# Kernel optimization log

Hardware: AMD Instinct MI355X
Metric: run time of the kernel (lower is better)

Reference implementation:

```python
import jax, jax.numpy as jnp
import numpy as np

IN, OUT, RANK, ALPHA, NSUB = 4096, 4096, 16, 32, 4
SCALING = ALPHA / RANK


def setup_inputs() -> dict:
    key = jax.random.key(0)
    ks = jax.random.split(key, 8)
    B, S = 4, 2048
    return {
        "x": jax.random.normal(ks[0], (B, S, IN), dtype=jnp.float32),
        "base_W": jax.random.normal(ks[1], (OUT, IN), dtype=jnp.float32) * 0.02,
        "base_b": jax.random.normal(ks[2], (OUT,), dtype=jnp.float32) * 0.02,
        "base_A": jax.random.normal(ks[3], (RANK, IN), dtype=jnp.float32) * 0.02,
        "base_B": jax.random.normal(ks[4], (OUT, RANK), dtype=jnp.float32) * 0.02,
        "sub_wgate": jax.random.normal(ks[5], (NSUB, IN), dtype=jnp.float32) * 0.02,
        "sub_A": jax.random.normal(ks[6], (NSUB, RANK, IN), dtype=jnp.float32) * 0.02,
        "sub_B": jax.random.normal(ks[7], (NSUB, OUT, RANK), dtype=jnp.float32) * 0.02,
    }


def reference(x, base_W, base_b, base_A, base_B, sub_wgate, sub_A, sub_B):
    # base linear: [B,S,IN] @ [IN,OUT] + bias
    out = jnp.einsum("bsd,od->bso", x, base_W) + base_b
    # base LoRA: x @ A^T @ B^T
    out = out + SCALING * jnp.einsum("bsr,or->bso", jnp.einsum("bsd,rd->bsr", x, base_A), base_B)
    # stacked ReLU-gated sub-adapters, batched over adapter dim j
    gates = jax.nn.relu(jnp.einsum("bsd,jd->bsj", x, sub_wgate))        # [B,S,J]
    mid = jnp.einsum("bsd,jrd->bsjr", x, sub_A)                           # [B,S,J,R] (small)
    # gate * (mid @ B^T) == (gate*mid) @ B^T since gate is per-token scalar
    gated_mid = mid * gates[..., None]
    out = out + SCALING * jnp.einsum("bsjr,jor->bso", gated_mid, sub_B)
    return out
```

## Files before the change

kernel.cpp:

```cpp
#include <hip/hip_runtime.h>
#include <hip/hip_bf16.h>
#include <stdint.h>

#define DIN   4096
#define DOUT  4096
#define RANK  16
#define NSUB  4
#define MTOT  8192
#define LDK   4160
#define KTAIL 64
#define NV    80
#define KTILES 65

typedef __attribute__((ext_vector_type(8)))  short    short8;
typedef __attribute__((ext_vector_type(4)))  float    floatx4;
typedef __attribute__((ext_vector_type(8)))  unsigned short ushort8;
typedef __attribute__((ext_vector_type(4)))  unsigned short ushort4v;

static __device__ __forceinline__ unsigned short f2bf(float f) {
    unsigned int u = __float_as_uint(f);
    unsigned int r = (u + 0x7FFFu + ((u >> 16) & 1u)) >> 16;
    return (unsigned short)r;
}

static __device__ __forceinline__ void async_copy16(const unsigned short* g, unsigned short* l) {
    __builtin_amdgcn_global_load_lds(
        (const __attribute__((address_space(1))) unsigned int*)g,
        (__attribute__((address_space(3))) unsigned int*)l,
        16, 0, 0);
}

__global__ __launch_bounds__(256) void build_v_kernel(
    const float* __restrict__ sub_wgate,
    const float* __restrict__ sub_A,
    unsigned short* __restrict__ Vc)
{
    const int t = threadIdx.x;
    const int row = blockIdx.x;
    const float* src = (row < 64) ? (sub_A + (size_t)row * DIN)
                     : (row < 68) ? (sub_wgate + (size_t)(row - 64) * DIN)
                     : nullptr;
#pragma unroll
    for (int i = 0; i < 4; ++i) {
        int c4 = t + 256 * i;
        ushort4v v;
        if (src) {
            float4 a = ((const float4*)src)[c4];
            v[0] = f2bf(a.x); v[1] = f2bf(a.y); v[2] = f2bf(a.z); v[3] = f2bf(a.w);
        } else {
            v[0] = v[1] = v[2] = v[3] = 0;
        }
        *(ushort4v*)(Vc + (size_t)row * DIN + c4 * 4) = v;
    }
}

__global__ __launch_bounds__(256) void convert_x_kernel(
    const float* __restrict__ x,
    unsigned short* __restrict__ Xc)
{
    const int t = threadIdx.x;
    const int b = blockIdx.x;
#pragma unroll
    for (int i = 0; i < 4; ++i) {
        const int row = b * 4 + i;
        const float4* s = (const float4*)(x + (size_t)row * DIN + t * 16);
        float4 a = s[0], b4 = s[1], c = s[2], d = s[3];
        ushort8 v0, v1;
        v0[0] = f2bf(a.x);  v0[1] = f2bf(a.y);  v0[2] = f2bf(a.z);  v0[3] = f2bf(a.w);
        v0[4] = f2bf(b4.x); v0[5] = f2bf(b4.y); v0[6] = f2bf(b4.z); v0[7] = f2bf(b4.w);
        v1[0] = f2bf(c.x);  v1[1] = f2bf(c.y);  v1[2] = f2bf(c.z);  v1[3] = f2bf(c.w);
        v1[4] = f2bf(d.x);  v1[5] = f2bf(d.y);  v1[6] = f2bf(d.z);  v1[7] = f2bf(d.w);
        unsigned short* o = Xc + (size_t)row * LDK + t * 16;
        *(ushort8*)o       = v0;
        *(ushort8*)(o + 8) = v1;
    }
}

#define XS_STG(P) do { unsigned short* d_ = &lds[(P)*8192 + t*8]; \
    _Pragma("unroll") for (int i_ = 0; i_ < 4; ++i_) \
        async_copy16(pXs + (size_t)(8*i_) * LDK, d_ + i_*2048); } while (0)
#define VS_STG(P) do { unsigned short* d_ = &lds[16384 + (P)*20480 + t*8]; \
    _Pragma("unroll") for (int i_ = 0; i_ < 10; ++i_) \
        async_copy16(pVs + (size_t)(8*i_) * DIN, d_ + i_*2048); } while (0)

#define XT_MM(P, KB) do { \
    short8 a0_ = *(const short8*)((const char*)lds + (P)*16384 + aB + (KB)); \
    short8 a1_ = *(const short8*)((const char*)lds + (P)*16384 + 8192 + aB + (KB)); \
    _Pragma("unroll") for (int n_ = 0; n_ < 5; ++n_) { \
        short8 b_ = *(const short8*)((const char*)lds + 32768 + (P)*40960 + n_*8192 + aB + (KB)); \
        acc[0][n_] = __builtin_amdgcn_mfma_f32_16x16x32_bf16(a0_, b_, acc[0][n_], 0, 0, 0); \
        acc[1][n_] = __builtin_amdgcn_mfma_f32_16x16x32_bf16(a1_, b_, acc[1][n_], 0, 0, 0); } \
} while (0)

#define XT_ITER(P, WN, DOSTG) do { \
    asm volatile("s_waitcnt vmcnt(" #WN ")" ::: "memory"); \
    asm volatile("s_barrier" ::: "memory"); \
    XT_MM(P, kb0); \
    XT_MM(P, kb1); \
    asm volatile("s_barrier" ::: "memory"); \
    if (DOSTG) { XS_STG(P); VS_STG(P); } \
    pXs += 256; pVs += 256; \
} while (0)

__global__ __launch_bounds__(256) void xtail_kernel(
    const unsigned short* __restrict__ Vc,
    unsigned short* __restrict__ Xc)
{
    __shared__ __align__(16) unsigned short lds[57344];

    const int t = threadIdx.x;
    const int l = t & 63;
    const int w = t >> 6;
    const int lane16 = l & 15;
    const int g = l >> 4;
    const int lx2 = lane16 & 7;
    const int m0 = blockIdx.x * 32;

    const int srow = t >> 5;
    const int scl  = (t & 31) ^ (srow & 7);
    const unsigned short* pXs = Xc + (size_t)(m0 + srow) * LDK + scl * 8;
    const unsigned short* pVs = Vc + (size_t)srow * DIN + scl * 8;

    const int hk  = lx2 >> 2;
    const int gx  = g ^ (lx2 & 3);
    const int kb0 = (((2*w + 0) ^ hk) * 4 + gx) * 16;
    const int kb1 = (((2*w + 1) ^ hk) * 4 + gx) * 16;
    const int aB  = lane16 * 512;

    floatx4 acc[2][5] = {};

    XS_STG(0); VS_STG(0); pXs += 256; pVs += 256;
    XS_STG(1); VS_STG(1); pXs += 256; pVs += 256;

#pragma unroll 1
    for (int c = 0; c < 14; c += 2) {
        XT_ITER(0, 14, 1);
        XT_ITER(1, 14, 1);
    }
    XT_ITER(0, 14, 0);
    XT_ITER(1, 0, 0);

    float* Pp = (float*)lds;
#pragma unroll
    for (int tm = 0; tm < 2; ++tm)
#pragma unroll
        for (int n = 0; n < 5; ++n)
#pragma unroll
            for (int r = 0; r < 4; ++r)
                Pp[((w * 32) + tm * 16 + (l >> 4) * 4 + r) * 80 + n * 16 + lane16] = acc[tm][n][r];
    __syncthreads();

#pragma unroll
    for (int i = 0; i < 8; ++i) {
        int v  = t + 256 * i;
        int tr = v >> 6;
        int c  = v & 63;
        int j  = c >> 4;
        float ps = 0.f, gs = 0.f;
#pragma unroll
        for (int q = 0; q < 4; ++q) {
            ps += Pp[(q * 32 + tr) * 80 + c];
            gs += Pp[(q * 32 + tr) * 80 + 64 + j];
        }
        Xc[(size_t)(m0 + tr) * LDK + DIN + c] = f2bf(2.0f * fmaxf(gs, 0.f) * ps);
    }
}

__global__ __launch_bounds__(256) void build_w_kernel(
    const float* __restrict__ W,
    const float* __restrict__ base_A,
    const float* __restrict__ base_B,
    const float* __restrict__ sub_B,
    unsigned short* __restrict__ Wc)
{
    __shared__ float bBs[8 * RANK];

    const int t  = threadIdx.x;
    const int o0 = (blockIdx.x >> 2) * 8;
    const int cc = (blockIdx.x & 3) * 1024;
    const int q  = (cc >> 2) + t;

    if (t < 128) bBs[t] = 2.0f * base_B[(size_t)o0 * RANK + t];
    __syncthreads();

    float4 acc[8];
#pragma unroll
    for (int o = 0; o < 8; ++o)
        acc[o] = ((const float4*)(W + (size_t)(o0 + o) * DIN))[q];

#pragma unroll
    for (int r = 0; r < RANK; ++r) {
        float4 a = ((const float4*)(base_A + (size_t)r * DIN))[q];
#pragma unroll
        for (int o = 0; o < 8; ++o) {
            float s = bBs[o * RANK + r];
            acc[o].x += s * a.x; acc[o].y += s * a.y;
            acc[o].z += s * a.z; acc[o].w += s * a.w;
        }
    }

#pragma unroll
    for (int o = 0; o < 8; ++o) {
        ushort4v v;
        v[0] = f2bf(acc[o].x); v[1] = f2bf(acc[o].y);
        v[2] = f2bf(acc[o].z); v[3] = f2bf(acc[o].w);
        *(ushort4v*)(Wc + (size_t)(o0 + o) * LDK + q * 4) = v;
    }

    if ((blockIdx.x & 3) == 0) {
#pragma unroll
        for (int i = 0; i < 2; ++i) {
            int v = t + 256 * i;
            int o = v >> 6;
            int c = v & 63;
            int j = c >> 4;
            int r = c & 15;
            float s = sub_B[((size_t)j * DOUT + (o0 + o)) * RANK + r];
            Wc[(size_t)(o0 + o) * LDK + DIN + c] = f2bf(s);
        }
    }
}

#define BARM() asm volatile("s_barrier" ::: "memory")

#define LDA_(B,MH,I,S) (*(const short8*)((const char*)lds + (B)*32768 + (MH)*8192 + (I)*2048 + (aBy ^ ((S)*64))))
#define LDB_(B,J,S)    (*(const short8*)((const char*)lds + 65536 + (B)*32768 + (J)*2048 + (bBy ^ ((S)*64))))

#define STG(P, DST) do { async_copy16((P), (DST)); \
                         async_copy16((P) + (size_t)64 * LDK, (DST) + 4096); } while (0)
#define STAGE_A0(P,B) STG((P), &lds[(B)*16384 + tid*8])
#define STAGE_A1(P,B) STG((P), &lds[(B)*16384 + 8192 + tid*8])
#define STAGE_B0(P,B) STG((P), &lds[32768 + (B)*16384 + tid*8])
#define STAGE_B1(P,B) STG((P), &lds[32768 + (B)*16384 + 8192 + tid*8])

#define MFMA_HALF(MH, JLO) do { \
    _Pragma("unroll") for (int s_ = 0; s_ < 2; ++s_) \
    _Pragma("unroll") for (int i_ = 0; i_ < 4; ++i_) \
    _Pragma("unroll") for (int jj_ = 0; jj_ < 2; ++jj_) \
        acc[(MH)*4+i_][(JLO)+jj_] = __builtin_amdgcn_mfma_f32_16x16x32_bf16( \
            af[i_][s_], bb[(JLO)+jj_][s_], acc[(MH)*4+i_][(JLO)+jj_], 0, 0, 0); \
} while (0)

#define TILE_BODY(T, CUR) do { \
     \
    _Pragma("unroll") for (int i_ = 0; i_ < 4; ++i_) { \
        af[i_][0] = LDA_(CUR, 0, i_, 0); af[i_][1] = LDA_(CUR, 0, i_, 1); } \
    _Pragma("unroll") for (int j_ = 0; j_ < 2; ++j_) { \
        bb[j_][0] = LDB_(CUR, j_, 0); bb[j_][1] = LDB_(CUR, j_, 1); } \
    if ((T) + 1 < KTILES) { STAGE_A1(pA1, (CUR) ^ 1); } \
    pA1 += 64; \
    __builtin_amdgcn_s_setprio(1); MFMA_HALF(0, 0); __builtin_amdgcn_s_setprio(0); \
    BARM(); \
     \
    _Pragma("unroll") for (int j_ = 2; j_ < 4; ++j_) { \
        bb[j_][0] = LDB_(CUR, j_, 0); bb[j_][1] = LDB_(CUR, j_, 1); } \
    __builtin_amdgcn_s_setprio(1); MFMA_HALF(0, 2); __builtin_amdgcn_s_setprio(0); \
    BARM(); \
     \
    _Pragma("unroll") for (int i_ = 0; i_ < 4; ++i_) { \
        af[i_][0] = LDA_(CUR, 1, i_, 0); af[i_][1] = LDA_(CUR, 1, i_, 1); } \
    if ((T) + 2 < KTILES) { STAGE_B0(pB0, CUR); STAGE_B1(pB1, CUR); } \
    pB0 += 64; pB1 += 64; \
    BARM(); \
    if ((T) + 2 < KTILES) { STAGE_A0(pA0, CUR); } \
    pA0 += 64; \
    __builtin_amdgcn_s_setprio(1); MFMA_HALF(1, 0); MFMA_HALF(1, 2); __builtin_amdgcn_s_setprio(0); \
    if ((T) + 2 < KTILES)      { asm volatile("s_waitcnt vmcnt(6)" ::: "memory"); } \
    else if ((T) + 1 < KTILES) { asm volatile("s_waitcnt vmcnt(0)" ::: "memory"); } \
    BARM(); \
} while (0)

__global__ __launch_bounds__(512, 2) void gemm_kernel(
    const unsigned short* __restrict__ Xc,
    const unsigned short* __restrict__ Wc,
    const float* __restrict__ bias,
    float* __restrict__ out)
{
    __shared__ unsigned short lds[65536];

    const int tid = threadIdx.x;
    const int l   = tid & 63;
    const int wv  = tid >> 6;
    const int wm  = wv >> 2;
    const int wn  = wv & 3;
    const int lane16 = l & 15;
    const int g   = l >> 4;
    const int lx  = lane16 & 7;

    const int bid = blockIdx.x;
    const int wg  = (bid & 7) * 64 + (bid >> 3);
    const int m0  = (wg >> 4) * 256;
    const int n0  = (wg & 15) * 256;

    const int aBy = wm * 16384 + lane16 * 128 + ((g ^ lx) << 4);
    const int bBy = wn * 8192  + lane16 * 128 + ((g ^ lx) << 4);

    const int r0 = tid >> 3;
    const int c0 = (tid & 7) ^ (r0 & 7);
    const unsigned short* pA0 = Xc + (size_t)(m0 + r0) * LDK + c0 * 8;
    const unsigned short* pA1 = pA0 + (size_t)128 * LDK;
    const unsigned short* pB0 = Wc + (size_t)(n0 + r0) * LDK + c0 * 8;
    const unsigned short* pB1 = pB0 + (size_t)128 * LDK;

    floatx4 acc[8][4] = {};
    short8 af[4][2], bb[4][2];

    STAGE_B0(pB0, 0); STAGE_B1(pB1, 0); STAGE_A0(pA0, 0); STAGE_A1(pA1, 0);
    STAGE_B0(pB0 + 64, 1); STAGE_B1(pB1 + 64, 1); STAGE_A0(pA0 + 64, 1);
    pA1 += 64; pB0 += 128; pB1 += 128; pA0 += 128;
    asm volatile("s_waitcnt vmcnt(6)" ::: "memory");
    BARM();

    for (int t = 0; t < KTILES - 1; t += 2) {
        TILE_BODY(t, 0);
        TILE_BODY(t + 1, 1);
    }
    TILE_BODY(KTILES - 1, 0);

    const int row_l = g * 4;
#pragma unroll
    for (int j = 0; j < 4; ++j) {
        const int gcol = n0 + wn * 64 + j * 16 + lane16;
        const float bv = bias[gcol];
#pragma unroll
        for (int i = 0; i < 8; ++i) {
            const int grow = m0 + wm * 128 + i * 16 + row_l;
            size_t base = (size_t)grow * DOUT + gcol;
            out[base]            = acc[i][j][0] + bv;
            out[base + DOUT]     = acc[i][j][1] + bv;
            out[base + 2 * DOUT] = acc[i][j][2] + bv;
            out[base + 3 * DOUT] = acc[i][j][3] + bv;
        }
    }
}

extern "C" void kernel_launch(void* const* d_in, const int* in_sizes, int n_in,
                              void* d_out, int out_size, void* d_ws, size_t ws_size,
                              hipStream_t stream) {
    const float* x         = (const float*)d_in[0];
    const float* base_W    = (const float*)d_in[1];
    const float* base_b    = (const float*)d_in[2];
    const float* base_A    = (const float*)d_in[3];
    const float* base_B    = (const float*)d_in[4];
    const float* sub_wgate = (const float*)d_in[5];
    const float* sub_A     = (const float*)d_in[6];
    const float* sub_B     = (const float*)d_in[7];
    float* out = (float*)d_out;

    unsigned short* Xc = (unsigned short*)d_ws;
    unsigned short* Wc = Xc + (size_t)MTOT * LDK;
    unsigned short* Vc = Wc + (size_t)DOUT * LDK;

    build_v_kernel<<<NV, 256, 0, stream>>>(sub_wgate, sub_A, Vc);
    convert_x_kernel<<<MTOT / 4, 256, 0, stream>>>(x, Xc);
    xtail_kernel<<<MTOT / 32, 256, 0, stream>>>(Vc, Xc);
    build_w_kernel<<<(DOUT / 8) * 4, 256, 0, stream>>>(base_W, base_A, base_B, sub_B, Wc);
    gemm_kernel<<<dim3(DOUT / 256 * (MTOT / 256)), 512, 0, stream>>>(Xc, Wc, base_b, out);
}
```

Measured before the change: 530.3 us.

## Merge prep kernels into one launch and restructure GEMM tile barrier schedule

New measurement: 528.4 us. No clear change (-0.4%).

```diff
diff --git a/kernel.cpp b/kernel.cpp
--- a/kernel.cpp
+++ b/kernel.cpp
@@ -30,49 +30,99 @@
         16, 0, 0);
 }
 
-__global__ __launch_bounds__(256) void build_v_kernel(
+__global__ __launch_bounds__(256) void prep_kernel(
+    const float* __restrict__ x,
+    unsigned short* __restrict__ Xc,
     const float* __restrict__ sub_wgate,
     const float* __restrict__ sub_A,
-    unsigned short* __restrict__ Vc)
+    unsigned short* __restrict__ Vc,
+    const float* __restrict__ W,
+    const float* __restrict__ base_A,
+    const float* __restrict__ base_B,
+    const float* __restrict__ sub_B,
+    unsigned short* __restrict__ Wc)
 {
+    __shared__ float bBs[8 * RANK];
     const int t = threadIdx.x;
-    const int row = blockIdx.x;
-    const float* src = (row < 64) ? (sub_A + (size_t)row * DIN)
-                     : (row < 68) ? (sub_wgate + (size_t)(row - 64) * DIN)
-                     : nullptr;
-#pragma unroll
-    for (int i = 0; i < 4; ++i) {
-        int c4 = t + 256 * i;
-        ushort4v v;
-        if (src) {
-            float4 a = ((const float4*)src)[c4];
-            v[0] = f2bf(a.x); v[1] = f2bf(a.y); v[2] = f2bf(a.z); v[3] = f2bf(a.w);
-        } else {
-            v[0] = v[1] = v[2] = v[3] = 0;
-        }
-        *(ushort4v*)(Vc + (size_t)row * DIN + c4 * 4) = v;
-    }
-}
-
-__global__ __launch_bounds__(256) void convert_x_kernel(
-    const float* __restrict__ x,
-    unsigned short* __restrict__ Xc)
-{
-    const int t = threadIdx.x;
-    const int b = blockIdx.x;
-#pragma unroll
-    for (int i = 0; i < 4; ++i) {
-        const int row = b * 4 + i;
-        const float4* s = (const float4*)(x + (size_t)row * DIN + t * 16);
-        float4 a = s[0], b4 = s[1], c = s[2], d = s[3];
-        ushort8 v0, v1;
-        v0[0] = f2bf(a.x);  v0[1] = f2bf(a.y);  v0[2] = f2bf(a.z);  v0[3] = f2bf(a.w);
-        v0[4] = f2bf(b4.x); v0[5] = f2bf(b4.y); v0[6] = f2bf(b4.z); v0[7] = f2bf(b4.w);
-        v1[0] = f2bf(c.x);  v1[1] = f2bf(c.y);  v1[2] = f2bf(c.z);  v1[3] = f2bf(c.w);
-        v1[4] = f2bf(d.x);  v1[5] = f2bf(d.y);  v1[6] = f2bf(d.z);  v1[7] = f2bf(d.w);
-        unsigned short* o = Xc + (size_t)row * LDK + t * 16;
-        *(ushort8*)o       = v0;
-        *(ushort8*)(o + 8) = v1;
+
+    if (blockIdx.x < 2048) {
+        const int b = blockIdx.x;
+#pragma unroll
+        for (int i = 0; i < 4; ++i) {
+            const int row = b * 4 + i;
+            const float4* s = (const float4*)(x + (size_t)row * DIN + t * 16);
+            float4 a = s[0], b4 = s[1], c = s[2], d = s[3];
+            ushort8 v0, v1;
+            v0[0] = f2bf(a.x);  v0[1] = f2bf(a.y);  v0[2] = f2bf(a.z);  v0[3] = f2bf(a.w);
+            v0[4] = f2bf(b4.x); v0[5] = f2bf(b4.y); v0[6] = f2bf(b4.z); v0[7] = f2bf(b4.w);
+            v1[0] = f2bf(c.x);  v1[1] = f2bf(c.y);  v1[2] = f2bf(c.z);  v1[3] = f2bf(c.w);
+            v1[4] = f2bf(d.x);  v1[5] = f2bf(d.y);  v1[6] = f2bf(d.z);  v1[7] = f2bf(d.w);
+            unsigned short* o = Xc + (size_t)row * LDK + t * 16;
+            *(ushort8*)o       = v0;
+            *(ushort8*)(o + 8) = v1;
+        }
+    } else if (blockIdx.x < 2048 + NV) {
+        const int row = blockIdx.x - 2048;
+        const float* src = (row < 64) ? (sub_A + (size_t)row * DIN)
+                         : (row < 68) ? (sub_wgate + (size_t)(row - 64) * DIN)
+                         : nullptr;
+#pragma unroll
+        for (int i = 0; i < 4; ++i) {
+            int c4 = t + 256 * i;
+            ushort4v v;
+            if (src) {
+                float4 a = ((const float4*)src)[c4];
+                v[0] = f2bf(a.x); v[1] = f2bf(a.y); v[2] = f2bf(a.z); v[3] = f2bf(a.w);
+            } else {
+                v[0] = v[1] = v[2] = v[3] = 0;
+            }
+            *(ushort4v*)(Vc + (size_t)row * DIN + c4 * 4) = v;
+        }
+    } else {
+        const int wb = blockIdx.x - 2048 - NV;
+        const int o0 = (wb >> 2) * 8;
+        const int cc = (wb & 3) * 1024;
+        const int q  = (cc >> 2) + t;
+
+        if (t < 128) bBs[t] = 2.0f * base_B[(size_t)o0 * RANK + t];
+        __syncthreads();
+
+        float4 acc[8];
+#pragma unroll
+        for (int o = 0; o < 8; ++o)
+            acc[o] = ((const float4*)(W + (size_t)(o0 + o) * DIN))[q];
+
+#pragma unroll
+        for (int r = 0; r < RANK; ++r) {
+            float4 a = ((const float4*)(base_A + (size_t)r * DIN))[q];
+#pragma unroll
+            for (int o = 0; o < 8; ++o) {
+                float s = bBs[o * RANK + r];
+                acc[o].x += s * a.x; acc[o].y += s * a.y;
+                acc[o].z += s * a.z; acc[o].w += s * a.w;
+            }
+        }
+
+#pragma unroll
+        for (int o = 0; o < 8; ++o) {
+            ushort4v v;
+            v[0] = f2bf(acc[o].x); v[1] = f2bf(acc[o].y);
+            v[2] = f2bf(acc[o].z); v[3] = f2bf(acc[o].w);
+            *(ushort4v*)(Wc + (size_t)(o0 + o) * LDK + q * 4) = v;
+        }
+
+        if ((wb & 3) == 0) {
+#pragma unroll
+            for (int i = 0; i < 2; ++i) {
+                int v = t + 256 * i;
+                int o = v >> 6;
+                int c = v & 63;
+                int j = c >> 4;
+                int r = c & 15;
+                float s = sub_B[((size_t)j * DOUT + (o0 + o)) * RANK + r];
+                Wc[(size_t)(o0 + o) * LDK + DIN + c] = f2bf(s);
+            }
+        }
     }
 }
 
@@ -166,61 +216,6 @@
     }
 }
 
-__global__ __launch_bounds__(256) void build_w_kernel(
-    const float* __restrict__ W,
-    const float* __restrict__ base_A,
-    const float* __restrict__ base_B,
-    const float* __restrict__ sub_B,
-    unsigned short* __restrict__ Wc)
-{
-    __shared__ float bBs[8 * RANK];
-
-    const int t  = threadIdx.x;
-    const int o0 = (blockIdx.x >> 2) * 8;
-    const int cc = (blockIdx.x & 3) * 1024;
-    const int q  = (cc >> 2) + t;
-
-    if (t < 128) bBs[t] = 2.0f * base_B[(size_t)o0 * RANK + t];
-    __syncthreads();
-
-    float4 acc[8];
-#pragma unroll
-    for (int o = 0; o < 8; ++o)
-        acc[o] = ((const float4*)(W + (size_t)(o0 + o) * DIN))[q];
-
-#pragma unroll
-    for (int r = 0; r < RANK; ++r) {
-        float4 a = ((const float4*)(base_A + (size_t)r * DIN))[q];
-#pragma unroll
-        for (int o = 0; o < 8; ++o) {
-            float s = bBs[o * RANK + r];
-            acc[o].x += s * a.x; acc[o].y += s * a.y;
-            acc[o].z += s * a.z; acc[o].w += s * a.w;
-        }
-    }
-
-#pragma unroll
-    for (int o = 0; o < 8; ++o) {
-        ushort4v v;
-        v[0] = f2bf(acc[o].x); v[1] = f2bf(acc[o].y);
-        v[2] = f2bf(acc[o].z); v[3] = f2bf(acc[o].w);
-        *(ushort4v*)(Wc + (size_t)(o0 + o) * LDK + q * 4) = v;
-    }
-
-    if ((blockIdx.x & 3) == 0) {
-#pragma unroll
-        for (int i = 0; i < 2; ++i) {
-            int v = t + 256 * i;
-            int o = v >> 6;
-            int c = v & 63;
-            int j = c >> 4;
-            int r = c & 15;
-            float s = sub_B[((size_t)j * DOUT + (o0 + o)) * RANK + r];
-            Wc[(size_t)(o0 + o) * LDK + DIN + c] = f2bf(s);
-        }
-    }
-}
-
 #define BARM() asm volatile("s_barrier" ::: "memory")
 
 #define LDA_(B,MH,I,S) (*(const short8*)((const char*)lds + (B)*32768 + (MH)*8192 + (I)*2048 + (aBy ^ ((S)*64))))
@@ -233,38 +228,34 @@
 #define STAGE_B0(P,B) STG((P), &lds[32768 + (B)*16384 + tid*8])
 #define STAGE_B1(P,B) STG((P), &lds[32768 + (B)*16384 + 8192 + tid*8])
 
-#define MFMA_HALF(MH, JLO) do { \
+#define MFMA_HALF2(MH) do { \
     _Pragma("unroll") for (int s_ = 0; s_ < 2; ++s_) \
     _Pragma("unroll") for (int i_ = 0; i_ < 4; ++i_) \
-    _Pragma("unroll") for (int jj_ = 0; jj_ < 2; ++jj_) \
-        acc[(MH)*4+i_][(JLO)+jj_] = __builtin_amdgcn_mfma_f32_16x16x32_bf16( \
-            af[i_][s_], bb[(JLO)+jj_][s_], acc[(MH)*4+i_][(JLO)+jj_], 0, 0, 0); \
+    _Pragma("unroll") for (int j_ = 0; j_ < 4; ++j_) \
+        acc[(MH)*4+i_][j_] = __builtin_amdgcn_mfma_f32_16x16x32_bf16( \
+            af[i_][s_], bb[j_][s_], acc[(MH)*4+i_][j_], 0, 0, 0); \
 } while (0)
 
 #define TILE_BODY(T, CUR) do { \
      \
     _Pragma("unroll") for (int i_ = 0; i_ < 4; ++i_) { \
         af[i_][0] = LDA_(CUR, 0, i_, 0); af[i_][1] = LDA_(CUR, 0, i_, 1); } \
-    _Pragma("unroll") for (int j_ = 0; j_ < 2; ++j_) { \
+    _Pragma("unroll") for (int j_ = 0; j_ < 4; ++j_) { \
         bb[j_][0] = LDB_(CUR, j_, 0); bb[j_][1] = LDB_(CUR, j_, 1); } \
-    if ((T) + 1 < KTILES) { STAGE_A1(pA1, (CUR) ^ 1); } \
-    pA1 += 64; \
-    __builtin_amdgcn_s_setprio(1); MFMA_HALF(0, 0); __builtin_amdgcn_s_setprio(0); \
+    asm volatile("s_waitcnt lgkmcnt(0)" ::: "memory"); \
+    __builtin_amdgcn_sched_barrier(0); \
     BARM(); \
      \
-    _Pragma("unroll") for (int j_ = 2; j_ < 4; ++j_) { \
-        bb[j_][0] = LDB_(CUR, j_, 0); bb[j_][1] = LDB_(CUR, j_, 1); } \
-    __builtin_amdgcn_s_setprio(1); MFMA_HALF(0, 2); __builtin_amdgcn_s_setprio(0); \
-    BARM(); \
+    if ((T) + 1 < KTILES) { STAGE_A1(pA1, (CUR) ^ 1); } \
+    if ((T) + 2 < KTILES) { STAGE_B0(pB0, CUR); STAGE_B1(pB1, CUR); } \
+    pA1 += 64; pB0 += 64; pB1 += 64; \
+    __builtin_amdgcn_s_setprio(1); MFMA_HALF2(0); __builtin_amdgcn_s_setprio(0); \
      \
     _Pragma("unroll") for (int i_ = 0; i_ < 4; ++i_) { \
         af[i_][0] = LDA_(CUR, 1, i_, 0); af[i_][1] = LDA_(CUR, 1, i_, 1); } \
-    if ((T) + 2 < KTILES) { STAGE_B0(pB0, CUR); STAGE_B1(pB1, CUR); } \
-    pB0 += 64; pB1 += 64; \
-    BARM(); \
     if ((T) + 2 < KTILES) { STAGE_A0(pA0, CUR); } \
     pA0 += 64; \
-    __builtin_amdgcn_s_setprio(1); MFMA_HALF(1, 0); MFMA_HALF(1, 2); __builtin_amdgcn_s_setprio(0); \
+    __builtin_amdgcn_s_setprio(1); MFMA_HALF2(1); __builtin_amdgcn_s_setprio(0); \
     if ((T) + 2 < KTILES)      { asm volatile("s_waitcnt vmcnt(6)" ::: "memory"); } \
     else if ((T) + 1 < KTILES) { asm volatile("s_waitcnt vmcnt(0)" ::: "memory"); } \
     BARM(); \
@@ -351,9 +342,8 @@
     unsigned short* Wc = Xc + (size_t)MTOT * LDK;
     unsigned short* Vc = Wc + (size_t)DOUT * LDK;
 
-    build_v_kernel<<<NV, 256, 0, stream>>>(sub_wgate, sub_A, Vc);
-    convert_x_kernel<<<MTOT / 4, 256, 0, stream>>>(x, Xc);
+    prep_kernel<<<2048 + NV + 2048, 256, 0, stream>>>(
+        x, Xc, sub_wgate, sub_A, Vc, base_W, base_A, base_B, sub_B, Wc);
     xtail_kernel<<<MTOT / 32, 256, 0, stream>>>(Vc, Xc);
-    build_w_kernel<<<(DOUT / 8) * 4, 256, 0, stream>>>(base_W, base_A, base_B, sub_B, Wc);
     gemm_kernel<<<dim3(DOUT / 256 * (MTOT / 256)), 512, 0, stream>>>(Xc, Wc, base_b, out);
 }
```
